# Kernel tuning notes

Hardware: AMD Instinct MI355X
Metric: run time of the kernel (lower is better)

The kernel has to match this reference:

```python
import jax, jax.numpy as jnp
import numpy as np

N = 10000   # nodes
E = 320000  # edges
B = 4       # batch
D = 128     # in_dim == out_dim
H = 4       # heads
DH = D // H # 32, per-head dim
OUT_L = D // H  # per-layer out_fc output dim (out_dim/num_heads)
NEG_SLOPE = 0.1


def setup_inputs() -> dict:
    key = jax.random.key(0)
    ks = jax.random.split(key, 20)
    inp = {
        "features": jax.random.normal(ks[0], (B, N, D), dtype=jnp.float32),
        "src": jax.random.randint(ks[1], (E,), 0, N),
        "dst": jax.random.randint(ks[2], (E,), 0, N),
        "edge_w": jax.random.uniform(ks[3], (E,), dtype=jnp.float32),
    }
    s = 0.05
    for l in range(2):
        k = 4 + 5 * l
        inp[f"fc_w{l}"] = jax.random.normal(ks[k], (D, D), dtype=jnp.float32) * s
        inp[f"al{l}"] = jax.random.normal(ks[k + 1], (H, DH), dtype=jnp.float32) * s
        inp[f"ar{l}"] = jax.random.normal(ks[k + 2], (H, DH), dtype=jnp.float32) * s
        inp[f"out_w{l}"] = jax.random.normal(ks[k + 3], (OUT_L, DH), dtype=jnp.float32) * s
        inp[f"out_b{l}"] = jnp.zeros((OUT_L,), dtype=jnp.float32)
    inp["mlp_w"] = jax.random.normal(ks[14], (D, 2 * D), dtype=jnp.float32) * s
    inp["mlp_b"] = jnp.zeros((D,), dtype=jnp.float32)
    return inp


def _gat_layer(x, src, dst, w, fc_w, al, ar, out_w, out_b):
    # x: [B,N,D]
    feat = jnp.einsum("bnd,ed->bne", x, fc_w).reshape(B, N, H, DH)  # fc, no bias
    el = jnp.einsum("bnhd,hd->bnh", feat, al)  # [B,N,H]
    er = jnp.einsum("bnhd,hd->bnh", feat, ar)
    # per-edge scores, edge-major: [E,B,H]
    e = jnp.moveaxis(el[:, src] + er[:, dst], 1, 0)
    e = jnp.where(e > 0, e, NEG_SLOPE * e)        # LeakyReLU(0.1)
    e = e * w[:, None, None]                      # edge weight applied pre-softmax
    # edge-softmax over incoming edges of each dst node
    m = jax.ops.segment_max(e, dst, num_segments=N)
    m = jnp.where(jnp.isfinite(m), m, 0.0)
    ex = jnp.exp(e - m[dst])
    den = jax.ops.segment_sum(ex, dst, num_segments=N)[dst]
    a = ex / jnp.where(den == 0, 1.0, den)        # [E,B,H]
    # u_mul_e + sum aggregation
    feat_n = jnp.moveaxis(feat, 0, 1)             # [N,B,H,DH]
    msg = feat_n[src] * a[..., None]              # [E,B,H,DH]
    agg = jax.ops.segment_sum(msg, dst, num_segments=N)  # [N,B,H,DH]
    out = jax.nn.relu(jnp.einsum("nbhd,od->nbho", agg, out_w) + out_b)
    # transpose(0,1) then concat heads along feature dim -> [B,N,H*OUT_L]
    return jnp.moveaxis(out, 0, 1).reshape(B, N, H * OUT_L)


def reference(features, src, dst, edge_w,
              fc_w0, al0, ar0, out_w0, out_b0,
              fc_w1, al1, ar1, out_w1, out_b1,
              mlp_w, mlp_b):
    x1 = _gat_layer(features, src, dst, edge_w, fc_w0, al0, ar0, out_w0, out_b0)
    x2 = _gat_layer(x1, src, dst, edge_w, fc_w1, al1, ar1, out_w1, out_b1)
    h = jnp.concatenate([x1, x2], axis=-1)        # [B,N,2*D]
    return jnp.einsum("bnk,ok->bno", h, mlp_w) + mlp_b  # eval mode: dropout off
```

## Files before the change

kernel.cpp:

```cpp
#include <hip/hip_runtime.h>
#include <hip/hip_fp16.h>
#include <float.h>

#define NN 10000
#define EE 320000
#define BB 4
#define DD 128
#define HH 4
#define DHH 32

union H4 { uint2 u2; __half2 h2[2]; };
union H8 { float4 f4; __half2 h2[4]; };

typedef _Float16 f16x8 __attribute__((ext_vector_type(8)));
typedef float f32x4 __attribute__((ext_vector_type(4)));

__global__ void pack_weights(const float* __restrict__ fc0, const float* __restrict__ fc1,
                             const float* __restrict__ mlp,
                             __half* __restrict__ bp0, __half* __restrict__ bp1,
                             __half* __restrict__ bpm,
                             int* __restrict__ cnt, int* __restrict__ cursor) {
    int s = blockIdx.x * 256 + threadIdx.x;
    int i = s & 7, l = (s >> 3) & 63, ct = (s >> 9) & 7, kt = s >> 12;
    int k = kt * 32 + 8 * (l >> 4) + i;
    int o = ct * 16 + (l & 15);
    bpm[s] = __float2half(mlp[o * 256 + k]);
    if (s < 16384) {
        bp0[s] = __float2half(fc0[o * 128 + k]);
        bp1[s] = __float2half(fc1[o * 128 + k]);
    }
    if (s < NN) { cnt[s] = 0; cursor[s] = 0; }
}

__global__ void count_edges(const int* __restrict__ dst, int* __restrict__ cnt) {
    int e = blockIdx.x * 256 + threadIdx.x;
    if (e < EE) atomicAdd(&cnt[dst[e]], 1);
}

__global__ void scan_kernel(const int* __restrict__ cnt, int* __restrict__ row_off) {
    __shared__ int part[1024];
    int t = threadIdx.x;
    const int CH = 10;
    int loc[CH];
    int s = 0;
#pragma unroll
    for (int j = 0; j < CH; ++j) {
        int i = t * CH + j;
        int v = (i < NN) ? cnt[i] : 0;
        loc[j] = s;
        s += v;
    }
    part[t] = s;
    __syncthreads();
    for (int off = 1; off < 1024; off <<= 1) {
        int v = (t >= off) ? part[t - off] : 0;
        __syncthreads();
        part[t] += v;
        __syncthreads();
    }
    int pre = (t > 0) ? part[t - 1] : 0;
#pragma unroll
    for (int j = 0; j < CH; ++j) {
        int i = t * CH + j;
        if (i < NN) row_off[i] = pre + loc[j];
    }
    if (t == 0) row_off[NN] = part[1023];
}

__global__ void scatter_edges(const int* __restrict__ dst, const int* __restrict__ row_off,
                              int* __restrict__ cursor, int* __restrict__ edge_ids) {
    int e = blockIdx.x * 256 + threadIdx.x;
    if (e < EE) {
        int d = dst[e];
        int p = atomicAdd(&cursor[d], 1);
        edge_ids[row_off[d] + p] = e;
    }
}

template <int K, bool A_HALF, bool HALF_OUT, bool BIAS>
__global__ __launch_bounds__(256) void mfma_gemm(
    const void* __restrict__ A_, int lda,
    const __half* __restrict__ Bp,
    const float* __restrict__ bias,
    __half* __restrict__ outh, float* __restrict__ outf, int ldo) {
    __shared__ __half A_s[64 * K];
    int tid = threadIdx.x;
    int row0 = blockIdx.x * 64;

    if (A_HALF) {
        const __half* A = (const __half*)A_;
#pragma unroll
        for (int it = 0; it < (64 * K / 8) / 256; ++it) {
            int s = it * 256 + tid;
            int r = s / (K / 8), c8 = s % (K / 8);
            uint4 v = *reinterpret_cast<const uint4*>(A + (size_t)(row0 + r) * lda + c8 * 8);
            int byte = (r * K + c8 * 8) * 2;
            byte ^= (r & 7) << 4;
            *reinterpret_cast<uint4*>((char*)A_s + byte) = v;
        }
    } else {
        const float* A = (const float*)A_;
#pragma unroll
        for (int it = 0; it < (64 * K / 4) / 256; ++it) {
            int s = it * 256 + tid;
            int r = s / (K / 4), c4 = s % (K / 4);
            float4 v = *reinterpret_cast<const float4*>(A + (size_t)(row0 + r) * lda + c4 * 4);
            __half h[4];
            h[0] = __float2half(v.x); h[1] = __float2half(v.y);
            h[2] = __float2half(v.z); h[3] = __float2half(v.w);
            int byte = (r * K + c4 * 4) * 2;
            byte ^= (r & 7) << 4;
            *reinterpret_cast<uint2*>((char*)A_s + byte) = *reinterpret_cast<uint2*>(h);
        }
    }
    __syncthreads();

    int l = tid & 63, w = tid >> 6;
    int g = l >> 4, r15 = l & 15;
    f32x4 acc[8] = {};

#pragma unroll
    for (int kt = 0; kt < K / 32; ++kt) {
        int row = w * 16 + r15;
        int byte = (row * K + kt * 32 + 8 * g) * 2;
        byte ^= (row & 7) << 4;
        f16x8 a = *reinterpret_cast<const f16x8*>((const char*)A_s + byte);
        const f16x8* bp = reinterpret_cast<const f16x8*>(Bp) + (size_t)(kt * 8) * 64 + l;
#pragma unroll
        for (int ct = 0; ct < 8; ++ct) {
            f16x8 b = bp[(size_t)ct * 64];
            acc[ct] = __builtin_amdgcn_mfma_f32_16x16x32_f16(a, b, acc[ct], 0, 0, 0);
        }
    }

#pragma unroll
    for (int ct = 0; ct < 8; ++ct) {
        int col = ct * 16 + r15;
#pragma unroll
        for (int reg = 0; reg < 4; ++reg) {
            int row = row0 + w * 16 + g * 4 + reg;
            float v = acc[ct][reg];
            if (BIAS) v += bias[col];
            if (HALF_OUT) outh[(size_t)row * ldo + col] = __float2half(v);
            else outf[(size_t)row * ldo + col] = v;
        }
    }
}

__global__ __launch_bounds__(256) void elr_kernel(
    const __half* __restrict__ feat_h, const float* __restrict__ al,
    const float* __restrict__ ar, float* __restrict__ el, float* __restrict__ er) {
    __shared__ float s_al[128], s_ar[128];
    int tid = threadIdx.x;
    if (tid < 128) s_al[tid] = al[tid];
    else s_ar[tid - 128] = ar[tid - 128];
    __syncthreads();
    int idx = blockIdx.x * 256 + tid;
    if (idx < BB * NN * HH) {
        int h = idx & 3;
        const __half* row = feat_h + (size_t)(idx >> 2) * 128 + h * 32;
        float al_acc = 0.f, ar_acc = 0.f;
#pragma unroll
        for (int q = 0; q < 8; ++q) {
            H4 u;
            u.u2 = *reinterpret_cast<const uint2*>(row + q * 4);
            float2 f0 = __half22float2(u.h2[0]);
            float2 f1 = __half22float2(u.h2[1]);
            int d = h * 32 + q * 4;
            al_acc += f0.x * s_al[d] + f0.y * s_al[d + 1] + f1.x * s_al[d + 2] + f1.y * s_al[d + 3];
            ar_acc += f0.x * s_ar[d] + f0.y * s_ar[d + 1] + f1.x * s_ar[d + 2] + f1.y * s_ar[d + 3];
        }
        el[idx] = al_acc;
        er[idx] = ar_acc;
    }
}

__global__ __launch_bounds__(256) void gat_aggregate(
    const int* __restrict__ row_off, const int* __restrict__ edge_ids,
    const int* __restrict__ src, const float* __restrict__ ew,
    const float* __restrict__ el, const float* __restrict__ er,
    const __half* __restrict__ feat_h, const float* __restrict__ out_w,
    const float* __restrict__ out_b, __half* __restrict__ hcat, int layer_off) {
    __shared__ float s_owt[32 * 33];
    __shared__ int s_srcA[4][64];
    __shared__ float s_wA[4][64];
    __shared__ float s_aggA[4][16 * 33];

    int tid = threadIdx.x;
    for (int i = tid; i < 1024; i += 256) {
        int o = i >> 5, d = i & 31;
        s_owt[d * 33 + o] = out_w[i];
    }
    __syncthreads();

    int wv = tid >> 6, lane = tid & 63;
    int n = blockIdx.x * 4 + wv;
    int start = row_off[n], end = row_off[n + 1];
    int* s_src = s_srcA[wv];
    float* s_w = s_wA[wv];
    float* s_agg = s_aggA[wv];

    int bh = lane & 15, sl = lane >> 4;
    int b = bh >> 2, h = bh & 3;
    const float* el_bh = el + (size_t)b * NN * 4 + h;
    float er1 = er[((size_t)b * NN + n) * 4 + h];
    const __half* fbase = feat_h + (size_t)b * NN * 128 + h * 32 + sl * 8;

    float den = 0.f;
    float acc8[8];
#pragma unroll
    for (int i = 0; i < 8; ++i) acc8[i] = 0.f;

    for (int base = start; base < end; base += 64) {
        int cnum = end - base;
        if (cnum > 64) cnum = 64;
        if (lane < cnum) {
            int eid = edge_ids[base + lane];
            s_src[lane] = src[eid];
            s_w[lane] = ew[eid];
        }
#pragma unroll 8
        for (int j = 0; j < cnum; ++j) {
            int s = s_src[j];
            float sc = el_bh[(size_t)s * 4] + er1;
            sc = sc > 0.f ? sc : 0.1f * sc;
            sc *= s_w[j];
            float p = __expf(sc);
            den += p;
            H8 u;
            u.f4 = *reinterpret_cast<const float4*>(fbase + (size_t)s * 128);
            float2 f0 = __half22float2(u.h2[0]);
            float2 f1 = __half22float2(u.h2[1]);
            float2 f2 = __half22float2(u.h2[2]);
            float2 f3 = __half22float2(u.h2[3]);
            acc8[0] += p * f0.x; acc8[1] += p * f0.y;
            acc8[2] += p * f1.x; acc8[3] += p * f1.y;
            acc8[4] += p * f2.x; acc8[5] += p * f2.y;
            acc8[6] += p * f3.x; acc8[7] += p * f3.y;
        }
    }

    float inv_den = (den == 0.f) ? 1.f : 1.f / den;
#pragma unroll
    for (int i = 0; i < 8; ++i) s_agg[bh * 33 + sl * 8 + i] = acc8[i] * inv_den;

    float o_acc[8];
#pragma unroll
    for (int i = 0; i < 8; ++i) o_acc[i] = out_b[sl * 8 + i];
#pragma unroll 8
    for (int dd = 0; dd < 32; ++dd) {
        float a = s_agg[bh * 33 + dd];
        const float* wr = s_owt + dd * 33 + sl * 8;
#pragma unroll
        for (int i = 0; i < 8; ++i) o_acc[i] += a * wr[i];
    }
    H8 ov;
#pragma unroll
    for (int k = 0; k < 4; ++k)
        ov.h2[k] = __floats2half2_rn(fmaxf(o_acc[2 * k], 0.f), fmaxf(o_acc[2 * k + 1], 0.f));
    *reinterpret_cast<float4*>(hcat + ((size_t)b * NN + n) * 256 + layer_off + h * 32 + sl * 8) = ov.f4;
}

extern "C" void kernel_launch(void* const* d_in, const int* in_sizes, int n_in,
                              void* d_out, int out_size, void* d_ws, size_t ws_size,
                              hipStream_t stream) {
    const float* features = (const float*)d_in[0];
    const int* src = (const int*)d_in[1];
    const int* dst = (const int*)d_in[2];
    const float* edge_w = (const float*)d_in[3];
    const float* fc_w0 = (const float*)d_in[4];
    const float* al0 = (const float*)d_in[5];
    const float* ar0 = (const float*)d_in[6];
    const float* out_w0 = (const float*)d_in[7];
    const float* out_b0 = (const float*)d_in[8];
    const float* fc_w1 = (const float*)d_in[9];
    const float* al1 = (const float*)d_in[10];
    const float* ar1 = (const float*)d_in[11];
    const float* out_w1 = (const float*)d_in[12];
    const float* out_b1 = (const float*)d_in[13];
    const float* mlp_w = (const float*)d_in[14];
    const float* mlp_b = (const float*)d_in[15];
    float* out = (float*)d_out;

    char* p = (char*)d_ws;
    auto take = [&](size_t bytes) {
        char* cur = p;
        p += (bytes + 255) & ~(size_t)255;
        return cur;
    };
    __half* bp0 = (__half*)take(16384 * 2);
    __half* bp1 = (__half*)take(16384 * 2);
    __half* bpm = (__half*)take(32768 * 2);
    __half* feat_h = (__half*)take((size_t)BB * NN * 128 * 2);
    __half* hcat = (__half*)take((size_t)BB * NN * 256 * 2);
    float* el = (float*)take((size_t)BB * NN * HH * 4);
    float* er = (float*)take((size_t)BB * NN * HH * 4);
    int* cnt = (int*)take((size_t)NN * 4);
    int* cursor = (int*)take((size_t)NN * 4);
    int* row_off = (int*)take((size_t)(NN + 1) * 4);
    int* edge_ids = (int*)take((size_t)EE * 4);
    (void)ws_size; (void)in_sizes; (void)n_in; (void)out_size;

    pack_weights<<<128, 256, 0, stream>>>(fc_w0, fc_w1, mlp_w, bp0, bp1, bpm, cnt, cursor);
    count_edges<<<EE / 256, 256, 0, stream>>>(dst, cnt);
    scan_kernel<<<1, 1024, 0, stream>>>(cnt, row_off);
    scatter_edges<<<EE / 256, 256, 0, stream>>>(dst, row_off, cursor, edge_ids);

    const int GEMM_GRID = (BB * NN) / 64;
    const int ELR_GRID = (BB * NN * HH + 255) / 256;
    const int AGG_GRID = NN / 4;

    mfma_gemm<128, false, true, false><<<GEMM_GRID, 256, 0, stream>>>(
        features, 128, bp0, nullptr, feat_h, nullptr, 128);
    elr_kernel<<<ELR_GRID, 256, 0, stream>>>(feat_h, al0, ar0, el, er);
    gat_aggregate<<<AGG_GRID, 256, 0, stream>>>(row_off, edge_ids, src, edge_w, el, er,
                                                feat_h, out_w0, out_b0, hcat, 0);
    mfma_gemm<128, true, true, false><<<GEMM_GRID, 256, 0, stream>>>(
        hcat, 256, bp1, nullptr, feat_h, nullptr, 128);
    elr_kernel<<<ELR_GRID, 256, 0, stream>>>(feat_h, al1, ar1, el, er);
    gat_aggregate<<<AGG_GRID, 256, 0, stream>>>(row_off, edge_ids, src, edge_w, el, er,
                                                feat_h, out_w1, out_b1, hcat, 128);
    mfma_gemm<256, true, false, true><<<GEMM_GRID, 256, 0, stream>>>(
        hcat, 256, bpm, mlp_b, nullptr, out, 128);
}
```

Before: 207.2 us.

## Store intermediates node-major so aggregation gathers one contiguous 1KB row per edge

The first GEMM now writes its output in [N,B] row order. The aggregation kernel can then fetch all 4 batches and 4 heads of a source node as one contiguous 1024-byte row, with each lane loading 16 bytes, and el/er are read as contiguous 16-float groups. The layer-1 GEMM keeps the node-major layout because hcat is written node-major, and the final MLP GEMM remaps rows back to [B,N] when storing to the output. The aim is better coalescing and cache-line use in the random gather, which dominates aggregation; the cost is scattered stores in the final GEMM epilogue.

```diff
diff --git a/kernel.cpp b/kernel.cpp
--- a/kernel.cpp
+++ b/kernel.cpp
@@ -14,6 +14,7 @@
 
 typedef _Float16 f16x8 __attribute__((ext_vector_type(8)));
 typedef float f32x4 __attribute__((ext_vector_type(4)));
+
 
 __global__ void pack_weights(const float* __restrict__ fc0, const float* __restrict__ fc1,
                              const float* __restrict__ mlp,
@@ -77,7 +78,7 @@
     }
 }
 
-template <int K, bool A_HALF, bool HALF_OUT, bool BIAS>
+template <int K, int REMAP, bool A_HALF, bool HALF_OUT, bool BIAS>
 __global__ __launch_bounds__(256) void mfma_gemm(
     const void* __restrict__ A_, int lda,
     const __half* __restrict__ Bp,
@@ -133,16 +134,23 @@
         }
     }
 
+    int grow[4];
+#pragma unroll
+    for (int reg = 0; reg < 4; ++reg) {
+        int r = row0 + w * 16 + g * 4 + reg;
+        if (REMAP == 0) grow[reg] = r;
+        else if (REMAP == 1) { int n = r % NN, b = r / NN; grow[reg] = n * 4 + b; }
+        else grow[reg] = (r & 3) * NN + (r >> 2);
+    }
 #pragma unroll
     for (int ct = 0; ct < 8; ++ct) {
         int col = ct * 16 + r15;
 #pragma unroll
         for (int reg = 0; reg < 4; ++reg) {
-            int row = row0 + w * 16 + g * 4 + reg;
             float v = acc[ct][reg];
             if (BIAS) v += bias[col];
-            if (HALF_OUT) outh[(size_t)row * ldo + col] = __float2half(v);
-            else outf[(size_t)row * ldo + col] = v;
+            if (HALF_OUT) outh[(size_t)grow[reg] * ldo + col] = __float2half(v);
+            else outf[(size_t)grow[reg] * ldo + col] = v;
         }
     }
 }
@@ -200,11 +208,10 @@
     float* s_w = s_wA[wv];
     float* s_agg = s_aggA[wv];
 
-    int bh = lane & 15, sl = lane >> 4;
-    int b = bh >> 2, h = bh & 3;
-    const float* el_bh = el + (size_t)b * NN * 4 + h;
-    float er1 = er[((size_t)b * NN + n) * 4 + h];
-    const __half* fbase = feat_h + (size_t)b * NN * 128 + h * 32 + sl * 8;
+    int bh4 = lane >> 2, sl = lane & 3;
+    float er1 = er[(size_t)n * 16 + bh4];
+    const float* el_base = el + bh4;
+    const __half* fbase = feat_h + lane * 8;
 
     float den = 0.f;
     float acc8[8];
@@ -222,13 +229,13 @@
 #pragma unroll 8
         for (int j = 0; j < cnum; ++j) {
             int s = s_src[j];
-            float sc = el_bh[(size_t)s * 4] + er1;
+            float sc = el_base[(size_t)s * 16] + er1;
             sc = sc > 0.f ? sc : 0.1f * sc;
             sc *= s_w[j];
             float p = __expf(sc);
             den += p;
             H8 u;
-            u.f4 = *reinterpret_cast<const float4*>(fbase + (size_t)s * 128);
+            u.f4 = *reinterpret_cast<const float4*>(fbase + (size_t)s * 512);
             float2 f0 = __half22float2(u.h2[0]);
             float2 f1 = __half22float2(u.h2[1]);
             float2 f2 = __half22float2(u.h2[2]);
@@ -242,14 +249,14 @@
 
     float inv_den = (den == 0.f) ? 1.f : 1.f / den;
 #pragma unroll
-    for (int i = 0; i < 8; ++i) s_agg[bh * 33 + sl * 8 + i] = acc8[i] * inv_den;
+    for (int i = 0; i < 8; ++i) s_agg[bh4 * 33 + sl * 8 + i] = acc8[i] * inv_den;
 
     float o_acc[8];
 #pragma unroll
     for (int i = 0; i < 8; ++i) o_acc[i] = out_b[sl * 8 + i];
 #pragma unroll 8
     for (int dd = 0; dd < 32; ++dd) {
-        float a = s_agg[bh * 33 + dd];
+        float a = s_agg[bh4 * 33 + dd];
         const float* wr = s_owt + dd * 33 + sl * 8;
 #pragma unroll
         for (int i = 0; i < 8; ++i) o_acc[i] += a * wr[i];
@@ -258,7 +265,8 @@
 #pragma unroll
     for (int k = 0; k < 4; ++k)
         ov.h2[k] = __floats2half2_rn(fmaxf(o_acc[2 * k], 0.f), fmaxf(o_acc[2 * k + 1], 0.f));
-    *reinterpret_cast<float4*>(hcat + ((size_t)b * NN + n) * 256 + layer_off + h * 32 + sl * 8) = ov.f4;
+    int b = bh4 >> 2, h = bh4 & 3;
+    *reinterpret_cast<float4*>(hcat + ((size_t)(n * 4 + b)) * 256 + layer_off + h * 32 + sl * 8) = ov.f4;
 }
 
 extern "C" void kernel_launch(void* const* d_in, const int* in_sizes, int n_in,
@@ -310,16 +318,16 @@
     const int ELR_GRID = (BB * NN * HH + 255) / 256;
     const int AGG_GRID = NN / 4;
 
-    mfma_gemm<128, false, true, false><<<GEMM_GRID, 256, 0, stream>>>(
+    mfma_gemm<128, 1, false, true, false><<<GEMM_GRID, 256, 0, stream>>>(
         features, 128, bp0, nullptr, feat_h, nullptr, 128);
     elr_kernel<<<ELR_GRID, 256, 0, stream>>>(feat_h, al0, ar0, el, er);
     gat_aggregate<<<AGG_GRID, 256, 0, stream>>>(row_off, edge_ids, src, edge_w, el, er,
                                                 feat_h, out_w0, out_b0, hcat, 0);
-    mfma_gemm<128, true, true, false><<<GEMM_GRID, 256, 0, stream>>>(
+    mfma_gemm<128, 0, true, true, false><<<GEMM_GRID, 256, 0, stream>>>(
         hcat, 256, bp1, nullptr, feat_h, nullptr, 128);
     elr_kernel<<<ELR_GRID, 256, 0, stream>>>(feat_h, al1, ar1, el, er);
     gat_aggregate<<<AGG_GRID, 256, 0, stream>>>(row_off, edge_ids, src, edge_w, el, er,
                                                 feat_h, out_w1, out_b1, hcat, 128);
-    mfma_gemm<256, true, false, true><<<GEMM_GRID, 256, 0, stream>>>(
+    mfma_gemm<256, 2, true, false, true><<<GEMM_GRID, 256, 0, stream>>>(
         hcat, 256, bpm, mlp_b, nullptr, out, 128);
 }
```

New measurement: 203.9 us. No clear change (-1.5%).

## Split aggregation per batch and process four edges in parallel per wave

Applied to the files above, without the earlier changes.

The GAT aggregation kernel now gives each block a single batch and four destination nodes, so the grid grows by a factor of four. Within a wave, lanes split into four edge slots, each covering 16 feature chunks across all 128 features. Partial sums are then reduced across slots with cross-lane shuffles. The aim is to cut the serial per-edge loop length and raise memory-level parallelism on the gathers. In exchange, edge ids, sources and edge weights are reloaded once per batch, and the shuffle-reduction step is new overhead.

```diff
diff --git a/kernel.cpp b/kernel.cpp
--- a/kernel.cpp
+++ b/kernel.cpp
@@ -14,6 +14,7 @@
 
 typedef _Float16 f16x8 __attribute__((ext_vector_type(8)));
 typedef float f32x4 __attribute__((ext_vector_type(4)));
+
 
 __global__ void pack_weights(const float* __restrict__ fc0, const float* __restrict__ fc1,
                              const float* __restrict__ mlp,
@@ -184,7 +185,7 @@
     __shared__ float s_owt[32 * 33];
     __shared__ int s_srcA[4][64];
     __shared__ float s_wA[4][64];
-    __shared__ float s_aggA[4][16 * 33];
+    __shared__ float s_aggA[4][132];
 
     int tid = threadIdx.x;
     for (int i = tid; i < 1024; i += 256) {
@@ -193,18 +194,22 @@
     }
     __syncthreads();
 
+    int g = blockIdx.x;
+    int b = (g & 7) >> 1;
+    int ngrp = ((g >> 3) << 1) | (g & 1);
     int wv = tid >> 6, lane = tid & 63;
-    int n = blockIdx.x * 4 + wv;
+    int n = ngrp * 4 + wv;
     int start = row_off[n], end = row_off[n + 1];
+
     int* s_src = s_srcA[wv];
     float* s_w = s_wA[wv];
     float* s_agg = s_aggA[wv];
 
-    int bh = lane & 15, sl = lane >> 4;
-    int b = bh >> 2, h = bh & 3;
-    const float* el_bh = el + (size_t)b * NN * 4 + h;
+    int e4 = lane >> 4, t = lane & 15;
+    int h = t >> 2;
+    const float* el_b = el + (size_t)b * NN * 4 + h;
     float er1 = er[((size_t)b * NN + n) * 4 + h];
-    const __half* fbase = feat_h + (size_t)b * NN * 128 + h * 32 + sl * 8;
+    const __half* fbase = feat_h + (size_t)b * NN * 128 + t * 8;
 
     float den = 0.f;
     float acc8[8];
@@ -219,10 +224,10 @@
             s_src[lane] = src[eid];
             s_w[lane] = ew[eid];
         }
-#pragma unroll 8
-        for (int j = 0; j < cnum; ++j) {
+#pragma unroll 4
+        for (int j = e4; j < cnum; j += 4) {
             int s = s_src[j];
-            float sc = el_bh[(size_t)s * 4] + er1;
+            float sc = el_b[(size_t)s * 4] + er1;
             sc = sc > 0.f ? sc : 0.1f * sc;
             sc *= s_w[j];
             float p = __expf(sc);
@@ -240,16 +245,26 @@
         }
     }
 
+    den += __shfl_xor(den, 16, 64);
+    den += __shfl_xor(den, 32, 64);
+#pragma unroll
+    for (int i = 0; i < 8; ++i) {
+        acc8[i] += __shfl_xor(acc8[i], 16, 64);
+        acc8[i] += __shfl_xor(acc8[i], 32, 64);
+    }
     float inv_den = (den == 0.f) ? 1.f : 1.f / den;
-#pragma unroll
-    for (int i = 0; i < 8; ++i) s_agg[bh * 33 + sl * 8 + i] = acc8[i] * inv_den;
-
+    if (e4 == 0) {
+#pragma unroll
+        for (int i = 0; i < 8; ++i) s_agg[t * 8 + i] = acc8[i] * inv_den;
+    }
+
+    int h3 = lane >> 4, sl = lane & 3;
     float o_acc[8];
 #pragma unroll
     for (int i = 0; i < 8; ++i) o_acc[i] = out_b[sl * 8 + i];
 #pragma unroll 8
     for (int dd = 0; dd < 32; ++dd) {
-        float a = s_agg[bh * 33 + dd];
+        float a = s_agg[h3 * 32 + dd];
         const float* wr = s_owt + dd * 33 + sl * 8;
 #pragma unroll
         for (int i = 0; i < 8; ++i) o_acc[i] += a * wr[i];
@@ -258,7 +273,7 @@
 #pragma unroll
     for (int k = 0; k < 4; ++k)
         ov.h2[k] = __floats2half2_rn(fmaxf(o_acc[2 * k], 0.f), fmaxf(o_acc[2 * k + 1], 0.f));
-    *reinterpret_cast<float4*>(hcat + ((size_t)b * NN + n) * 256 + layer_off + h * 32 + sl * 8) = ov.f4;
+    *reinterpret_cast<float4*>(hcat + ((size_t)b * NN + n) * 256 + layer_off + h3 * 32 + sl * 8) = ov.f4;
 }
 
 extern "C" void kernel_launch(void* const* d_in, const int* in_sizes, int n_in,
@@ -308,7 +323,7 @@
 
     const int GEMM_GRID = (BB * NN) / 64;
     const int ELR_GRID = (BB * NN * HH + 255) / 256;
-    const int AGG_GRID = NN / 4;
+    const int AGG_GRID = NN;
 
     mfma_gemm<128, false, true, false><<<GEMM_GRID, 256, 0, stream>>>(
         features, 128, bp0, nullptr, feat_h, nullptr, 128);
```

After: 237.9 us. 14.8% more time.
